# Kernel tuning notes

Hardware: AMD Instinct MI355X
Metric: run time of the kernel (lower is better)

The kernel has to match this reference:

```python
import jax, jax.numpy as jnp
import numpy as np

B, S, D, H = 2, 2048, 1024, 16
DK = D // H


def setup_inputs() -> dict:
    key = jax.random.key(0)
    ks = jax.random.split(key, 12)
    init = lambda k, shp: (jax.random.normal(k, shp, dtype=jnp.float32) * 0.02)
    return {
        'query': jax.random.normal(ks[0], (B, S, D), dtype=jnp.float32),
        'key_in': jax.random.normal(ks[1], (B, S, D), dtype=jnp.float32),
        'value': jax.random.normal(ks[2], (B, S, D), dtype=jnp.float32),
        'w_q': init(ks[3], (D, D)), 'b_q': jnp.zeros((D,), jnp.float32),
        'w_k': init(ks[4], (D, D)), 'b_k': jnp.zeros((D,), jnp.float32),
        'w_v': init(ks[5], (D, D)), 'b_v': jnp.zeros((D,), jnp.float32),
        'w_o': init(ks[6], (D, D)), 'b_o': jnp.zeros((D,), jnp.float32),
        'fuzzy_centers': jax.random.normal(ks[7], (H, 3), dtype=jnp.float32),
        'fuzzy_widths': jnp.ones((H, 3), jnp.float32),
        'temperature': jnp.ones((1,), jnp.float32),
    }


def reference(query, key_in, value, w_q, b_q, w_k, b_k, w_v, b_v, w_o, b_o,
              fuzzy_centers, fuzzy_widths, temperature):
    b, s, d = query.shape
    h, dk = H, DK
    proj = lambda x, w, bias: x @ w.T + bias
    # [b,s,d] -> [b,h,s,dk]
    Q = proj(query, w_q, b_q).reshape(b, s, h, dk).transpose(0, 2, 1, 3)
    K = proj(key_in, w_k, b_k).reshape(b, s, h, dk).transpose(0, 2, 1, 3)
    V = proj(value, w_v, b_v).reshape(b, s, h, dk).transpose(0, 2, 1, 3)
    scores = jnp.einsum('bhsd,bhtd->bhst', Q, K) / np.sqrt(dk).astype(np.float32)
    # Faithful to torch: every (head,func) gaussian is applied to ALL heads' scores,
    # so each score gets sum of h*3 memberships, divided by 3.
    c = fuzzy_centers.reshape(-1)
    w = fuzzy_widths.reshape(-1)
    fz = jnp.zeros_like(scores)
    for i in range(h * 3):  # small fixed loop over membership functions
        fz = fz + jnp.exp(-(scores - c[i]) ** 2 / (2.0 * w[i] ** 2))
    fz = (fz / 3.0) / temperature[0]
    attn = jax.nn.softmax(fz, axis=-1)
    attended = jnp.einsum('bhst,bhtd->bhsd', attn, V)
    attended = attended.transpose(0, 2, 1, 3).reshape(b, s, d)
    return attended @ w_o.T + b_o
```

## Files before the change

kernel.cpp:

```cpp
#include <hip/hip_runtime.h>
#include <hip/hip_bf16.h>


#define S_LEN 2048
#define DMODEL 1024
#define NHEAD 16
#define DKH 64
#define NLUT 2048
#define LUT_MIN (-10.0f)
#define LUT_MAX (10.0f)

typedef __attribute__((ext_vector_type(8))) short bfx8;
typedef __attribute__((ext_vector_type(4))) float fx4;
typedef __attribute__((ext_vector_type(16))) float fx16;
typedef __attribute__((ext_vector_type(4))) unsigned ux4;

__device__ __forceinline__ short f2bf(float x) {
    unsigned u = __builtin_bit_cast(unsigned, x);
    u = (u + 0x7fffu + ((u >> 16) & 1u)) >> 16;
    return (short)u;
}

__device__ __forceinline__ unsigned cvt_pk_bf16(float lo, float hi) {
    unsigned r;
    asm("v_cvt_pk_bf16_f32 %0, %1, %2" : "=v"(r) : "v"(lo), "v"(hi));
    return r;
}

__device__ __forceinline__ void plane_swap(unsigned& a, unsigned& b) {
    asm volatile("v_permlane32_swap_b32 %0, %1" : "+v"(a), "+v"(b));
}

__device__ __forceinline__ void stage8_f32(const float* __restrict__ src, short* dst) {
    float4 a = *(const float4*)(src);
    float4 b = *(const float4*)(src + 4);
    bfx8 r;
    r[0] = f2bf(a.x); r[1] = f2bf(a.y); r[2] = f2bf(a.z); r[3] = f2bf(a.w);
    r[4] = f2bf(b.x); r[5] = f2bf(b.y); r[6] = f2bf(b.z); r[7] = f2bf(b.w);
    *(bfx8*)dst = r;
}

__device__ __forceinline__ void gload_lds16(const void* g, void* l) {
    __builtin_amdgcn_global_load_lds(
        (const __attribute__((address_space(1))) unsigned int*)g,
        (__attribute__((address_space(3))) unsigned int*)l, 16, 0, 0);
}

__device__ void lut_body(const float* __restrict__ centers, const float* __restrict__ widths,
                         const float* __restrict__ temp, unsigned* __restrict__ lutp) {
    __shared__ float fzb[NLUT];
    __shared__ float red[256];
    __shared__ float cs[48], wsb[48];
    int tid = threadIdx.x;
    if (tid < 48) { cs[tid] = centers[tid]; wsb[tid] = widths[tid]; }
    __syncthreads();
    float invT = 1.0f / temp[0];
    const float step = (LUT_MAX - LUT_MIN) / (float)(NLUT - 1);
    float lmax = -1e30f;
    for (int i = tid; i < NLUT; i += 256) {
        float s = LUT_MIN + step * (float)i;
        float fz = 0.0f;
        #pragma unroll 1
        for (int j = 0; j < 48; j++) {
            float d = s - cs[j];
            float w = wsb[j];
            fz += expf(-(d * d) / (2.0f * w * w));
        }
        fz = fz * (1.0f / 3.0f) * invT;
        fzb[i] = fz;
        lmax = fmaxf(lmax, fz);
    }
    red[tid] = lmax;
    __syncthreads();
    for (int off = 128; off > 0; off >>= 1) {
        if (tid < off) red[tid] = fmaxf(red[tid], red[tid + off]);
        __syncthreads();
    }
    float m = red[0];
    __syncthreads();
    for (int i = tid; i < NLUT; i += 256) fzb[i] = expf(fzb[i] - m);
    __syncthreads();
    for (int i = tid; i < NLUT; i += 256) {
        float g0 = fzb[i];
        float g1 = fzb[(i + 1 < NLUT) ? i + 1 : NLUT - 1];
        unsigned lo = (unsigned short)f2bf(g0);
        unsigned hi = (unsigned short)f2bf(g1);
        lutp[i] = lo | (hi << 16);
    }
}

__global__ void build_lut_pk(const float* centers, const float* widths,
                             const float* temp, unsigned* lutp) {
    lut_body(centers, widths, temp, lutp);
}

__global__ void cast_bf16(const float* __restrict__ src, short* __restrict__ dst, int n8) {
    int i = blockIdx.x * 256 + threadIdx.x;
    if (i < n8) stage8_f32(src + (size_t)i * 8, dst + (size_t)i * 8);
}

__global__ void prep_all(const float* q, const float* kin, const float* v,
        const float* wq, const float* wk, const float* wv, const float* wo,
        short* xq, short* xk, short* xv,
        short* bwq, short* bwk, short* bwv, short* bwo,
        const float* centers, const float* widths, const float* temp,
        unsigned* lutp) {
    int bid = blockIdx.x;
    if (bid >= 8192) {
        lut_body(centers, widths, temp, lutp);
        return;
    }
    const float* src; short* dst; int blk;
    if (bid < 6144) {
        int y = bid >> 11; blk = bid & 2047;
        src = (y == 0) ? q : (y == 1) ? kin : v;
        dst = (y == 0) ? xq : (y == 1) ? xk : xv;
    } else {
        int y = (bid - 6144) >> 9; blk = (bid - 6144) & 511;
        src = (y == 0) ? wq : (y == 1) ? wk : (y == 2) ? wv : wo;
        dst = (y == 0) ? bwq : (y == 1) ? bwk : (y == 2) ? bwv : bwo;
    }
    size_t i = (size_t)blk * 256 + threadIdx.x;
    stage8_f32(src + i * 8, (short*)dst + i * 8);
}

struct GemmJob {
    const short* A; const short* W; const float* bias;
    short* obf; float* of32; int mode; float scale;
};

__global__ __launch_bounds__(256, 2) void gemm128(GemmJob j0, GemmJob j1, GemmJob j2) {
    __shared__ __align__(16) short As[128 * 32];
    __shared__ __align__(16) short Bs[128 * 32];
    GemmJob jb = (blockIdx.z == 0) ? j0 : (blockIdx.z == 1) ? j1 : j2;
    int tid = threadIdx.x, wave = tid >> 6, lane = tid & 63, quad = lane >> 4, l15 = lane & 15;
    int m0 = blockIdx.y * 128, n0 = blockIdx.x * 128;
    int wm = (wave >> 1) * 64, wn = (wave & 1) * 64;

    fx4 acc[4][4];
    #pragma unroll
    for (int i = 0; i < 4; i++)
        #pragma unroll
        for (int j = 0; j < 4; j++)
            #pragma unroll
            for (int r = 0; r < 4; r++) acc[i][j][r] = 0.0f;

    int fc = (quad ^ ((l15 >> 1) & 3)) * 8;

    for (int k0 = 0; k0 < DMODEL; k0 += 32) {
        __syncthreads();
        #pragma unroll
        for (int r = 0; r < 2; r++) {
            int slot = r * 256 + wave * 64 + lane;
            int row = slot >> 2, c = slot & 3, gc = c ^ ((row >> 1) & 3);
            gload_lds16(jb.A + (size_t)(m0 + row) * DMODEL + k0 + gc * 8,
                        &As[(r * 256 + wave * 64) * 8]);
            gload_lds16(jb.W + (size_t)(n0 + row) * DMODEL + k0 + gc * 8,
                        &Bs[(r * 256 + wave * 64) * 8]);
        }
        __syncthreads();
        bfx8 af[4], bfr[4];
        #pragma unroll
        for (int i = 0; i < 4; i++) af[i] = *(const bfx8*)(&As[(wm + i * 16 + l15) * 32 + fc]);
        #pragma unroll
        for (int j = 0; j < 4; j++) bfr[j] = *(const bfx8*)(&Bs[(wn + j * 16 + l15) * 32 + fc]);
        #pragma unroll
        for (int i = 0; i < 4; i++)
            #pragma unroll
            for (int j = 0; j < 4; j++)
                acc[i][j] = __builtin_amdgcn_mfma_f32_16x16x32_bf16(af[i], bfr[j], acc[i][j], 0, 0, 0);
    }

    #pragma unroll
    for (int j = 0; j < 4; j++) {
        int n = n0 + wn + j * 16 + l15;
        float bv = jb.bias[n];
        #pragma unroll
        for (int i = 0; i < 4; i++) {
            #pragma unroll
            for (int r = 0; r < 4; r++) {
                int m = m0 + wm + i * 16 + quad * 4 + r;
                float v = (acc[i][j][r] + bv) * jb.scale;
                if (jb.mode == 0) {
                    int b = m >> 11, s = m & 2047, h = n >> 6, dk = n & 63;
                    jb.obf[(((size_t)(b * NHEAD + h)) * S_LEN + s) * DKH + dk] = f2bf(v);
                } else if (jb.mode == 1) {
                    int b = m >> 11, s = m & 2047, h = n >> 6, dk = n & 63;
                    jb.obf[(((size_t)(b * NHEAD + h)) * DKH + dk) * S_LEN + s] = f2bf(v);
                } else {
                    jb.of32[(size_t)m * DMODEL + n] = v;
                }
            }
        }
    }
}

__global__ __launch_bounds__(256, 4) void flash_fuzzy(const short* __restrict__ Qb,
        const short* __restrict__ Kb, const short* __restrict__ VTb,
        const unsigned* __restrict__ lutg, short* __restrict__ AO) {
    __shared__ __align__(16) short Ks[64 * 64];
    __shared__ __align__(16) short Vs[64 * 64];
    __shared__ unsigned lut[NLUT];

    int tid = threadIdx.x, wave = tid >> 6, lane = tid & 63;
    int l31 = lane & 31, hi = lane >> 5;
    int wq = wave >> 1, st = wave & 1;
    int q0 = blockIdx.x * 64, bh = blockIdx.y;
    const short* Qp = Qb + (size_t)bh * S_LEN * DKH;
    const short* Kp = Kb + (size_t)bh * S_LEN * DKH;
    const short* Vp = VTb + (size_t)bh * DKH * S_LEN;

    #pragma unroll
    for (int i = tid; i < NLUT / 4; i += 256)
        ((uint4*)lut)[i] = ((const uint4*)lutg)[i];

    bfx8 aq[4];
    #pragma unroll
    for (int ks = 0; ks < 4; ks++)
        aq[ks] = *(const bfx8*)(Qp + (size_t)(q0 + wq * 32 + l31) * DKH + ks * 16 + hi * 8);

    fx16 oacc[2];
    #pragma unroll
    for (int dt = 0; dt < 2; dt++)
        #pragma unroll
        for (int r = 0; r < 16; r++) oacc[dt][r] = 0.0f;
    float den = 0.0f;

    const float invh = (float)(NLUT - 1) / (LUT_MAX - LUT_MIN);
    const float xoff = -LUT_MIN * invh;

    int srow[2], sgc[2];
    #pragma unroll
    for (int r = 0; r < 2; r++) {
        int slot = (wave * 2 + r) * 64 + lane;
        srow[r] = slot >> 3;
        sgc[r] = (slot & 7) ^ (srow[r] & 7);
    }

    for (int t0 = 0; t0 < S_LEN; t0 += 64) {
        __syncthreads();
        #pragma unroll
        for (int r = 0; r < 2; r++) {
            gload_lds16(Kp + (size_t)(t0 + srow[r]) * DKH + sgc[r] * 8,
                        &Ks[((wave * 2 + r) * 64) * 8]);
            gload_lds16(Vp + (size_t)srow[r] * S_LEN + t0 + sgc[r] * 8,
                        &Vs[((wave * 2 + r) * 64) * 8]);
        }
        __syncthreads();

        fx16 sac;
        #pragma unroll
        for (int r = 0; r < 16; r++) sac[r] = 0.0f;
        {
            int row = st * 32 + l31;
            #pragma unroll
            for (int ks = 0; ks < 4; ks++) {
                bfx8 kf = *(const bfx8*)(&Ks[row * 64 + (((ks * 2 + hi) ^ (row & 7)) * 8)]);
                sac = __builtin_amdgcn_mfma_f32_32x32x16_bf16(kf, aq[ks], sac, 0, 0, 0);
            }
        }

        unsigned w[8];
        #pragma unroll
        for (int t = 0; t < 8; t++) {
            float pv[2];
            #pragma unroll
            for (int u = 0; u < 2; u++) {
                float s = sac[t * 2 + u];
                float x = fmaf(s, invh, xoff);
                x = fminf(fmaxf(x, 0.0f), (float)(NLUT - 1));
                int j = (int)x;
                float f = x - (float)j;
                unsigned pr = lut[j];
                float v0 = __builtin_bit_cast(float, pr << 16);
                float v1 = __builtin_bit_cast(float, pr & 0xffff0000u);
                pv[u] = fmaf(f, v1 - v0, v0);
            }
            w[t] = cvt_pk_bf16(pv[0], pv[1]);
        }
        #pragma unroll
        for (int t = 0; t < 8; t++) {
            den += __builtin_bit_cast(float, w[t] << 16);
            den += __builtin_bit_cast(float, w[t] & 0xffff0000u);
        }

        plane_swap(w[0], w[2]); plane_swap(w[1], w[3]);
        plane_swap(w[4], w[6]); plane_swap(w[5], w[7]);
        ux4 b0v = {w[0], w[1], w[2], w[3]};
        ux4 b1v = {w[4], w[5], w[6], w[7]};
        bfx8 pb0 = __builtin_bit_cast(bfx8, b0v);
        bfx8 pb1 = __builtin_bit_cast(bfx8, b1v);

        #pragma unroll
        for (int dt = 0; dt < 2; dt++) {
            int row = dt * 32 + l31;
            bfx8 v0f = *(const bfx8*)(&Vs[row * 64 + (((st * 4 + 0 + hi) ^ (row & 7)) * 8)]);
            bfx8 v1f = *(const bfx8*)(&Vs[row * 64 + (((st * 4 + 2 + hi) ^ (row & 7)) * 8)]);
            oacc[dt] = __builtin_amdgcn_mfma_f32_32x32x16_bf16(v0f, pb0, oacc[dt], 0, 0, 0);
            oacc[dt] = __builtin_amdgcn_mfma_f32_32x32x16_bf16(v1f, pb1, oacc[dt], 0, 0, 0);
        }
    }

    den += __shfl_xor(den, 32);

    __syncthreads();
    float* obuf = (wq == 0) ? (float*)Ks : (float*)Vs;
    float* dbuf = (float*)lut;
    if (st == 1) {
        #pragma unroll
        for (int dt = 0; dt < 2; dt++)
            #pragma unroll
            for (int r = 0; r < 16; r++)
                obuf[(dt * 16 + r) * 64 + lane] = oacc[dt][r];
        dbuf[wq * 64 + lane] = den;
    }
    __syncthreads();
    if (st == 0) {
        float dtot = den + dbuf[wq * 64 + lane];
        int b = bh >> 4, h = bh & 15;
        #pragma unroll
        for (int dt = 0; dt < 2; dt++) {
            #pragma unroll
            for (int r = 0; r < 16; r++) {
                float o = oacc[dt][r] + obuf[(dt * 16 + r) * 64 + lane];
                int dk = dt * 32 + (r & 3) + 8 * (r >> 2) + 4 * hi;
                int q = q0 + wq * 32 + l31;
                AO[((size_t)(b * S_LEN + q)) * DMODEL + h * DKH + dk] = f2bf(o / dtot);
            }
        }
    }
}

extern "C" void kernel_launch(void* const* d_in, const int* in_sizes, int n_in,
                              void* d_out, int out_size, void* d_ws, size_t ws_size,
                              hipStream_t stream) {
    const float* query   = (const float*)d_in[0];
    const float* key_in  = (const float*)d_in[1];
    const float* value   = (const float*)d_in[2];
    const float* w_q     = (const float*)d_in[3];
    const float* b_q     = (const float*)d_in[4];
    const float* w_k     = (const float*)d_in[5];
    const float* b_k     = (const float*)d_in[6];
    const float* w_v     = (const float*)d_in[7];
    const float* b_v     = (const float*)d_in[8];
    const float* w_o     = (const float*)d_in[9];
    const float* b_o     = (const float*)d_in[10];
    const float* centers = (const float*)d_in[11];
    const float* widths  = (const float*)d_in[12];
    const float* temp    = (const float*)d_in[13];

    char* p = (char*)d_ws;
    auto alloc = [&](size_t bytes) -> void* {
        void* r = (void*)p;
        p += (bytes + 255) & ~(size_t)255;
        return r;
    };
    const size_t nBHSD = (size_t)2 * NHEAD * S_LEN * DKH;
    const size_t nW    = (size_t)DMODEL * DMODEL;
    unsigned* lutp = (unsigned*)alloc(NLUT * 4);
    short* Qb  = (short*)alloc(nBHSD * 2);
    short* Kb  = (short*)alloc(nBHSD * 2);
    short* VTb = (short*)alloc(nBHSD * 2);

    char* save = p;
    short* xq  = (short*)alloc(nBHSD * 2);
    short* xk  = (short*)alloc(nBHSD * 2);
    short* xv  = (short*)alloc(nBHSD * 2);
    short* bwq = (short*)alloc(nW * 2);
    short* bwk = (short*)alloc(nW * 2);
    short* bwv = (short*)alloc(nW * 2);
    short* bwo = (short*)alloc(nW * 2);
    bool fused = ((size_t)(p - (char*)d_ws) <= ws_size);

    dim3 blk(256);
    dim3 gq(8, 32, 3), g1(8, 32, 1), fg(32, 32);
    GemmJob JO;

    if (fused) {
        short* AO = xq;
        prep_all<<<dim3(8193), blk, 0, stream>>>(query, key_in, value, w_q, w_k, w_v, w_o,
                xq, xk, xv, bwq, bwk, bwv, bwo, centers, widths, temp, lutp);
        GemmJob JQ = {xq, bwq, b_q, Qb,  nullptr, 0, 0.125f};
        GemmJob JK = {xk, bwk, b_k, Kb,  nullptr, 0, 1.0f};
        GemmJob JV = {xv, bwv, b_v, VTb, nullptr, 1, 1.0f};
        gemm128<<<gq, blk, 0, stream>>>(JQ, JK, JV);
        flash_fuzzy<<<fg, blk, 0, stream>>>(Qb, Kb, VTb, lutp, AO);
        JO = {AO, bwo, b_o, nullptr, (float*)d_out, 2, 1.0f};
        gemm128<<<g1, blk, 0, stream>>>(JO, JO, JO);
    } else {
        p = save;
        short* xf = (short*)alloc(nBHSD * 2);
        short* wb = (short*)alloc(nW * 2);
        short* AO = xf;
        const int n8x = (int)(nBHSD / 8), n8w = (int)(nW / 8);
        dim3 cg((n8x + 255) / 256), cw((n8w + 255) / 256);
        build_lut_pk<<<dim3(1), blk, 0, stream>>>(centers, widths, temp, lutp);
        cast_bf16<<<cg, blk, 0, stream>>>(query, xf, n8x);
        cast_bf16<<<cw, blk, 0, stream>>>(w_q, wb, n8w);
        JO = {xf, wb, b_q, Qb, nullptr, 0, 0.125f};
        gemm128<<<g1, blk, 0, stream>>>(JO, JO, JO);
        cast_bf16<<<cg, blk, 0, stream>>>(key_in, xf, n8x);
        cast_bf16<<<cw, blk, 0, stream>>>(w_k, wb, n8w);
        JO = {xf, wb, b_k, Kb, nullptr, 0, 1.0f};
        gemm128<<<g1, blk, 0, stream>>>(JO, JO, JO);
        cast_bf16<<<cg, blk, 0, stream>>>(value, xf, n8x);
        cast_bf16<<<cw, blk, 0, stream>>>(w_v, wb, n8w);
        JO = {xf, wb, b_v, VTb, nullptr, 1, 1.0f};
        gemm128<<<g1, blk, 0, stream>>>(JO, JO, JO);
        flash_fuzzy<<<fg, blk, 0, stream>>>(Qb, Kb, VTb, lutp, AO);
        cast_bf16<<<cw, blk, 0, stream>>>(w_o, wb, n8w);
        JO = {AO, wb, b_o, nullptr, (float*)d_out, 2, 1.0f};
        gemm128<<<g1, blk, 0, stream>>>(JO, JO, JO);
    }
}
```

Before: 306.6 us.

## Double-buffer LDS tiles in GEMM and fuzzy flash-attention loops

Both the projection GEMM and the fuzzy flash-attention kernel now keep two LDS buffers. The next K-slice or K/V tile is prefetched with async global-to-LDS loads while the current one is consumed by MFMAs, so each iteration needs one barrier instead of two. The goal is to hide global load latency behind compute. In exchange, LDS use doubles per block: about 40KB per flash block at 4 blocks per CU. That could limit occupancy, and the barrier still has to wait for the prefetch to land.

```diff
diff --git a/kernel.cpp b/kernel.cpp
--- a/kernel.cpp
+++ b/kernel.cpp
@@ -130,8 +130,8 @@
 };
 
 __global__ __launch_bounds__(256, 2) void gemm128(GemmJob j0, GemmJob j1, GemmJob j2) {
-    __shared__ __align__(16) short As[128 * 32];
-    __shared__ __align__(16) short Bs[128 * 32];
+    __shared__ __align__(16) short As[2][128 * 32];
+    __shared__ __align__(16) short Bs[2][128 * 32];
     GemmJob jb = (blockIdx.z == 0) ? j0 : (blockIdx.z == 1) ? j1 : j2;
     int tid = threadIdx.x, wave = tid >> 6, lane = tid & 63, quad = lane >> 4, l15 = lane & 15;
     int m0 = blockIdx.y * 128, n0 = blockIdx.x * 128;
@@ -147,28 +147,41 @@
 
     int fc = (quad ^ ((l15 >> 1) & 3)) * 8;
 
+    int srow[2], sgc[2];
+    #pragma unroll
+    for (int r = 0; r < 2; r++) {
+        int slot = r * 256 + wave * 64 + lane;
+        srow[r] = slot >> 2;
+        sgc[r] = (slot & 3) ^ ((srow[r] >> 1) & 3);
+    }
+
+    auto stage = [&](int k0, int buf) {
+        #pragma unroll
+        for (int r = 0; r < 2; r++) {
+            gload_lds16(jb.A + (size_t)(m0 + srow[r]) * DMODEL + k0 + sgc[r] * 8,
+                        &As[buf][(r * 256 + wave * 64) * 8]);
+            gload_lds16(jb.W + (size_t)(n0 + srow[r]) * DMODEL + k0 + sgc[r] * 8,
+                        &Bs[buf][(r * 256 + wave * 64) * 8]);
+        }
+    };
+
+    stage(0, 0);
+    __syncthreads();
+    int buf = 0;
     for (int k0 = 0; k0 < DMODEL; k0 += 32) {
-        __syncthreads();
-        #pragma unroll
-        for (int r = 0; r < 2; r++) {
-            int slot = r * 256 + wave * 64 + lane;
-            int row = slot >> 2, c = slot & 3, gc = c ^ ((row >> 1) & 3);
-            gload_lds16(jb.A + (size_t)(m0 + row) * DMODEL + k0 + gc * 8,
-                        &As[(r * 256 + wave * 64) * 8]);
-            gload_lds16(jb.W + (size_t)(n0 + row) * DMODEL + k0 + gc * 8,
-                        &Bs[(r * 256 + wave * 64) * 8]);
-        }
-        __syncthreads();
+        if (k0 + 32 < DMODEL) stage(k0 + 32, buf ^ 1);
         bfx8 af[4], bfr[4];
         #pragma unroll
-        for (int i = 0; i < 4; i++) af[i] = *(const bfx8*)(&As[(wm + i * 16 + l15) * 32 + fc]);
-        #pragma unroll
-        for (int j = 0; j < 4; j++) bfr[j] = *(const bfx8*)(&Bs[(wn + j * 16 + l15) * 32 + fc]);
+        for (int i = 0; i < 4; i++) af[i] = *(const bfx8*)(&As[buf][(wm + i * 16 + l15) * 32 + fc]);
+        #pragma unroll
+        for (int j = 0; j < 4; j++) bfr[j] = *(const bfx8*)(&Bs[buf][(wn + j * 16 + l15) * 32 + fc]);
         #pragma unroll
         for (int i = 0; i < 4; i++)
             #pragma unroll
             for (int j = 0; j < 4; j++)
                 acc[i][j] = __builtin_amdgcn_mfma_f32_16x16x32_bf16(af[i], bfr[j], acc[i][j], 0, 0, 0);
+        __syncthreads();
+        buf ^= 1;
     }
 
     #pragma unroll
@@ -198,8 +211,8 @@
 __global__ __launch_bounds__(256, 4) void flash_fuzzy(const short* __restrict__ Qb,
         const short* __restrict__ Kb, const short* __restrict__ VTb,
         const unsigned* __restrict__ lutg, short* __restrict__ AO) {
-    __shared__ __align__(16) short Ks[64 * 64];
-    __shared__ __align__(16) short Vs[64 * 64];
+    __shared__ __align__(16) short Ks[2][64 * 64];
+    __shared__ __align__(16) short Vs[2][64 * 64];
     __shared__ unsigned lut[NLUT];
 
     int tid = threadIdx.x, wave = tid >> 6, lane = tid & 63;
@@ -210,25 +223,6 @@
     const short* Kp = Kb + (size_t)bh * S_LEN * DKH;
     const short* Vp = VTb + (size_t)bh * DKH * S_LEN;
 
-    #pragma unroll
-    for (int i = tid; i < NLUT / 4; i += 256)
-        ((uint4*)lut)[i] = ((const uint4*)lutg)[i];
-
-    bfx8 aq[4];
-    #pragma unroll
-    for (int ks = 0; ks < 4; ks++)
-        aq[ks] = *(const bfx8*)(Qp + (size_t)(q0 + wq * 32 + l31) * DKH + ks * 16 + hi * 8);
-
-    fx16 oacc[2];
-    #pragma unroll
-    for (int dt = 0; dt < 2; dt++)
-        #pragma unroll
-        for (int r = 0; r < 16; r++) oacc[dt][r] = 0.0f;
-    float den = 0.0f;
-
-    const float invh = (float)(NLUT - 1) / (LUT_MAX - LUT_MIN);
-    const float xoff = -LUT_MIN * invh;
-
     int srow[2], sgc[2];
     #pragma unroll
     for (int r = 0; r < 2; r++) {
@@ -236,17 +230,41 @@
         srow[r] = slot >> 3;
         sgc[r] = (slot & 7) ^ (srow[r] & 7);
     }
-
-    for (int t0 = 0; t0 < S_LEN; t0 += 64) {
-        __syncthreads();
+    auto stage = [&](int t0, int buf) {
         #pragma unroll
         for (int r = 0; r < 2; r++) {
             gload_lds16(Kp + (size_t)(t0 + srow[r]) * DKH + sgc[r] * 8,
-                        &Ks[((wave * 2 + r) * 64) * 8]);
+                        &Ks[buf][((wave * 2 + r) * 64) * 8]);
             gload_lds16(Vp + (size_t)srow[r] * S_LEN + t0 + sgc[r] * 8,
-                        &Vs[((wave * 2 + r) * 64) * 8]);
-        }
-        __syncthreads();
+                        &Vs[buf][((wave * 2 + r) * 64) * 8]);
+        }
+    };
+
+    stage(0, 0);
+
+    #pragma unroll
+    for (int i = tid; i < NLUT / 4; i += 256)
+        ((uint4*)lut)[i] = ((const uint4*)lutg)[i];
+
+    bfx8 aq[4];
+    #pragma unroll
+    for (int ks = 0; ks < 4; ks++)
+        aq[ks] = *(const bfx8*)(Qp + (size_t)(q0 + wq * 32 + l31) * DKH + ks * 16 + hi * 8);
+
+    fx16 oacc[2];
+    #pragma unroll
+    for (int dt = 0; dt < 2; dt++)
+        #pragma unroll
+        for (int r = 0; r < 16; r++) oacc[dt][r] = 0.0f;
+    float den = 0.0f;
+
+    const float invh = (float)(NLUT - 1) / (LUT_MAX - LUT_MIN);
+    const float xoff = -LUT_MIN * invh;
+
+    __syncthreads();
+    int buf = 0;
+    for (int t0 = 0; t0 < S_LEN; t0 += 64) {
+        if (t0 + 64 < S_LEN) stage(t0 + 64, buf ^ 1);
 
         fx16 sac;
         #pragma unroll
@@ -255,7 +273,7 @@
             int row = st * 32 + l31;
             #pragma unroll
             for (int ks = 0; ks < 4; ks++) {
-                bfx8 kf = *(const bfx8*)(&Ks[row * 64 + (((ks * 2 + hi) ^ (row & 7)) * 8)]);
+                bfx8 kf = *(const bfx8*)(&Ks[buf][row * 64 + (((ks * 2 + hi) ^ (row & 7)) * 8)]);
                 sac = __builtin_amdgcn_mfma_f32_32x32x16_bf16(kf, aq[ks], sac, 0, 0, 0);
             }
         }
@@ -294,17 +312,19 @@
         #pragma unroll
         for (int dt = 0; dt < 2; dt++) {
             int row = dt * 32 + l31;
-            bfx8 v0f = *(const bfx8*)(&Vs[row * 64 + (((st * 4 + 0 + hi) ^ (row & 7)) * 8)]);
-            bfx8 v1f = *(const bfx8*)(&Vs[row * 64 + (((st * 4 + 2 + hi) ^ (row & 7)) * 8)]);
+            bfx8 v0f = *(const bfx8*)(&Vs[buf][row * 64 + (((st * 4 + 0 + hi) ^ (row & 7)) * 8)]);
+            bfx8 v1f = *(const bfx8*)(&Vs[buf][row * 64 + (((st * 4 + 2 + hi) ^ (row & 7)) * 8)]);
             oacc[dt] = __builtin_amdgcn_mfma_f32_32x32x16_bf16(v0f, pb0, oacc[dt], 0, 0, 0);
             oacc[dt] = __builtin_amdgcn_mfma_f32_32x32x16_bf16(v1f, pb1, oacc[dt], 0, 0, 0);
         }
+
+        __syncthreads();
+        buf ^= 1;
     }
 
     den += __shfl_xor(den, 32);
 
-    __syncthreads();
-    float* obuf = (wq == 0) ? (float*)Ks : (float*)Vs;
+    float* obuf = (float*)Ks + wq * 2048;
     float* dbuf = (float*)lut;
     if (st == 1) {
         #pragma unroll
```

Result: no change. 308.3 us (+0.5%).
